# Kernel tuning notes

Hardware: AMD Instinct MI355X
Metric: run time of the kernel (lower is better)

Reference implementation:

```python
import jax, jax.numpy as jnp
import numpy as np

N = 50000          # nodes
E_RAND = 800000    # random edges (avg degree 16)
IN, HID, HEADS, OUT = 256, 64, 4, 40
NEG_SLOPE = 0.2    # PyG GATConv default leaky_relu slope
BN_EPS = 1e-5


def setup_inputs() -> dict:
    key = jax.random.key(0)
    ks = jax.random.split(key, 24)
    x = jax.random.normal(ks[0], (N, IN), jnp.float32)
    ei = jax.random.randint(ks[1], (2, E_RAND), 0, N)
    loops = jnp.arange(N, dtype=ei.dtype)
    edge_index = jnp.concatenate([ei, jnp.stack([loops, loops])], axis=1)  # add self loops (PyG default)
    s = 0.1
    d = {
        "x": x,
        "edge_index": edge_index,
        "W0": jax.random.normal(ks[2], (IN, HEADS * HID), jnp.float32) * s,
        "a_src0": jax.random.normal(ks[3], (HEADS, HID), jnp.float32) * s,
        "a_dst0": jax.random.normal(ks[4], (HEADS, HID), jnp.float32) * s,
        "b0": jax.random.normal(ks[5], (HEADS * HID,), jnp.float32) * s,
        "bn0_g": jnp.ones((HEADS * HID,), jnp.float32),
        "bn0_b": jnp.zeros((HEADS * HID,), jnp.float32),
        "bn0_m": jax.random.normal(ks[6], (HEADS * HID,), jnp.float32) * s,
        "bn0_v": jax.random.uniform(ks[7], (HEADS * HID,), jnp.float32, 0.5, 1.5),
        "W1": jax.random.normal(ks[8], (HEADS * HID, HEADS * HID), jnp.float32) * s,
        "a_src1": jax.random.normal(ks[9], (HEADS, HID), jnp.float32) * s,
        "a_dst1": jax.random.normal(ks[10], (HEADS, HID), jnp.float32) * s,
        "b1": jax.random.normal(ks[11], (HEADS * HID,), jnp.float32) * s,
        "bn1_g": jnp.ones((HEADS * HID,), jnp.float32),
        "bn1_b": jnp.zeros((HEADS * HID,), jnp.float32),
        "bn1_m": jax.random.normal(ks[12], (HEADS * HID,), jnp.float32) * s,
        "bn1_v": jax.random.uniform(ks[13], (HEADS * HID,), jnp.float32, 0.5, 1.5),
        "W2": jax.random.normal(ks[14], (HEADS * HID, OUT), jnp.float32) * s,
        "a_src2": jax.random.normal(ks[15], (1, OUT), jnp.float32) * s,
        "a_dst2": jax.random.normal(ks[16], (1, OUT), jnp.float32) * s,
        "b2": jax.random.normal(ks[17], (OUT,), jnp.float32) * s,
    }
    return d


def gat_conv(x, edge_index, W, att_src, att_dst, heads, ch):
    """PyG GATConv (eval mode): gather -> leaky_relu attn -> segment softmax -> scatter add."""
    src, dst = edge_index[0], edge_index[1]
    h = (x @ W).reshape(-1, heads, ch)                       # [N,H,C]
    a_s = jnp.einsum('nhc,hc->nh', h, att_src)
    a_d = jnp.einsum('nhc,hc->nh', h, att_dst)
    e = jax.nn.leaky_relu(a_s[src] + a_d[dst], NEG_SLOPE)    # [E,H]
    m = jax.ops.segment_max(e, dst, num_segments=N)
    m = jax.lax.stop_gradient(jnp.where(jnp.isfinite(m), m, 0.0))
    p = jnp.exp(e - m[dst])
    denom = jax.ops.segment_sum(p, dst, num_segments=N)
    alpha = p / (denom[dst] + 1e-16)                         # [E,H]
    msg = h[src] * alpha[:, :, None]                         # [E,H,C]
    return jax.ops.segment_sum(msg, dst, num_segments=N)     # [N,H,C]


def _bn(h, g, b, m, v):
    return g * (h - m) * jax.lax.rsqrt(v + BN_EPS) + b


def reference(x, edge_index, W0, a_src0, a_dst0, b0, bn0_g, bn0_b, bn0_m, bn0_v,
              W1, a_src1, a_dst1, b1, bn1_g, bn1_b, bn1_m, bn1_v,
              W2, a_src2, a_dst2, b2):
    h = gat_conv(x, edge_index, W0, a_src0, a_dst0, HEADS, HID).reshape(N, HEADS * HID) + b0
    h = jax.nn.elu(_bn(h, bn0_g, bn0_b, bn0_m, bn0_v))
    h = gat_conv(h, edge_index, W1, a_src1, a_dst1, HEADS, HID).reshape(N, HEADS * HID) + b1
    h = jax.nn.elu(_bn(h, bn1_g, bn1_b, bn1_m, bn1_v))
    out = gat_conv(h, edge_index, W2, a_src2, a_dst2, 1, OUT).reshape(N, OUT) + b2
    return out
```

## Files before the change

### kernel.cpp

```cpp
#include <hip/hip_runtime.h>
#include <cstdint>
#include <cstddef>

constexpr int kN = 50000;
constexpr float kSlope = 0.2f;
constexpr float kBnEps = 1e-5f;

static inline int ceil_div(int a, int b) { return (a + b - 1) / b; }

typedef __attribute__((ext_vector_type(8))) _Float16 half8;
typedef __attribute__((ext_vector_type(8))) unsigned short ushortx8;
typedef __attribute__((ext_vector_type(4))) float f32x4;

__device__ inline unsigned short f2h_us(float f) {
  _Float16 h = (_Float16)f;
  return *(unsigned short*)&h;
}

__device__ inline void gload16(const void* g, void* l) {
  __builtin_amdgcn_global_load_lds((const __attribute__((address_space(1))) unsigned int*)g,
                                   (__attribute__((address_space(3))) unsigned int*)l, 16, 0, 0);
}


__global__ void k_prep_degree(const int* __restrict__ dst, int* __restrict__ deg, int E,
                              const float* __restrict__ x, unsigned short* __restrict__ x16,
                              const float* __restrict__ W0, unsigned short* __restrict__ Wt0,
                              const float* __restrict__ W1, unsigned short* __restrict__ Wt1,
                              const float* __restrict__ W2, unsigned short* __restrict__ Wt2) {
  const int tid = blockIdx.x * blockDim.x + threadIdx.x;
  const int nthr = gridDim.x * blockDim.x;
  for (int e = tid; e < E; e += nthr) atomicAdd(&deg[dst[e]], 1);
  const int N4 = kN * 64;
  const int S0 = 256 * 256, S1 = 256 * 256, S2 = 128 * 256;
  const int total = N4 + S0 + S1 + S2;
  for (int i = tid; i < total; i += nthr) {
    if (i < N4) {
      float4 v = ((const float4*)x)[i];
      ushort4 o;
      o.x = f2h_us(v.x);
      o.y = f2h_us(v.y);
      o.z = f2h_us(v.z);
      o.w = f2h_us(v.w);
      ((ushort4*)x16)[i] = o;
    } else {
      int j = i - N4;
      if (j < S0) {
        int nc = j >> 8, k = j & 255;
        Wt0[j] = f2h_us(W0[(size_t)k * 256 + nc]);
      } else if (j < S0 + S1) {
        int t = j - S0;
        int nc = t >> 8, k = t & 255;
        Wt1[t] = f2h_us(W1[(size_t)k * 256 + nc]);
      } else {
        int t = j - S0 - S1;
        int nc = t >> 8, k = t & 255;
        Wt2[t] = (nc < 40) ? f2h_us(W2[(size_t)k * 40 + nc]) : (unsigned short)0;
      }
    }
  }
}


__global__ void k_scan1(const int* __restrict__ deg, int* __restrict__ rp,
                        int* __restrict__ bsum, int n) {
  __shared__ int sm[256];
  int i = blockIdx.x * 256 + threadIdx.x;
  int v = (i < n) ? deg[i] : 0;
  sm[threadIdx.x] = v;
  __syncthreads();
  for (int off = 1; off < 256; off <<= 1) {
    int t = (threadIdx.x >= off) ? sm[threadIdx.x - off] : 0;
    __syncthreads();
    sm[threadIdx.x] += t;
    __syncthreads();
  }
  if (i < n) rp[i + 1] = sm[threadIdx.x];
  if (threadIdx.x == 255) bsum[blockIdx.x] = sm[255];
}

__global__ void k_scan2(int* bsum, int nb) {
  __shared__ int sm[256];
  int v = (threadIdx.x < nb) ? bsum[threadIdx.x] : 0;
  sm[threadIdx.x] = v;
  __syncthreads();
  for (int off = 1; off < 256; off <<= 1) {
    int t = (threadIdx.x >= off) ? sm[threadIdx.x - off] : 0;
    __syncthreads();
    sm[threadIdx.x] += t;
    __syncthreads();
  }
  if (threadIdx.x < nb) bsum[threadIdx.x] = sm[threadIdx.x] - v;
}

__global__ void k_scan3(int* __restrict__ rp, const int* __restrict__ bsum, int n) {
  int i = blockIdx.x * 256 + threadIdx.x;
  if (i < n) rp[i + 1] += bsum[blockIdx.x];
  if (i == 0) rp[0] = 0;
}


__device__ __forceinline__ void gemm_body(
    int bx, int by, const unsigned short* __restrict__ A, const unsigned short* __restrict__ Bt,
    unsigned short* __restrict__ C, const float* __restrict__ asrc,
    const float* __restrict__ adst, float* __restrict__ a_s, float* __restrict__ a_d, int M,
    int K, int Nc, int ldc, int heads, int acols) {
  constexpr int BM = 128, BK = 32;
  __shared__ unsigned short As[BM * BK];
  __shared__ unsigned short Bs[BM * BK];
  int tid = threadIdx.x;
  int wave = tid >> 6, lane = tid & 63;
  int quad = lane >> 4, l16 = lane & 15;
  int wm = (wave & 1) * 64, wn = (wave >> 1) * 64;
  int bm = bx * BM, bn = by * BM;
  int srow = lane >> 2;
  int spart = lane & 3;
  f32x4 acc[4][4] = {};
  for (int k0 = 0; k0 < K; k0 += BK) {
#pragma unroll
    for (int it = 0; it < 2; it++) {
      int chunk = wave * 2 + it;
      int row = chunk * 16 + srow;
      gload16(A + (size_t)(bm + row) * K + k0 + spart * 8, As + chunk * 512);
      gload16(Bt + (size_t)(bn + row) * K + k0 + spart * 8, Bs + chunk * 512);
    }
    __syncthreads();
    half8 af[4], bf[4];
#pragma unroll
    for (int i = 0; i < 4; i++) {
      af[i] = *(const half8*)(As + (wm + i * 16 + l16) * BK + quad * 8);
      bf[i] = *(const half8*)(Bs + (wn + i * 16 + l16) * BK + quad * 8);
    }
#pragma unroll
    for (int i = 0; i < 4; i++)
#pragma unroll
      for (int j = 0; j < 4; j++)
        acc[i][j] = __builtin_amdgcn_mfma_f32_16x16x32_f16(af[i], bf[j], acc[i][j], 0, 0, 0);
    __syncthreads();
  }
#pragma unroll
  for (int i = 0; i < 4; i++) {
#pragma unroll
    for (int j = 0; j < 4; j++) {
      int col = bn + wn + j * 16 + l16;
      if (col >= Nc) continue;
#pragma unroll
      for (int r = 0; r < 4; r++) {
        int row = bm + wm + i * 16 + quad * 4 + r;
        if (row < M) C[(size_t)row * ldc + col] = f2h_us(acc[i][j][r]);
      }
    }
  }
  int ghead = (bn + wn) >> 6;
  if (ghead < heads) {
    float asv[4], adv[4];
#pragma unroll
    for (int j = 0; j < 4; j++) {
      int col = bn + wn + j * 16 + l16;
      bool ok = col < acols;
      asv[j] = ok ? asrc[col] : 0.f;
      adv[j] = ok ? adst[col] : 0.f;
    }
#pragma unroll
    for (int i = 0; i < 4; i++) {
#pragma unroll
      for (int r = 0; r < 4; r++) {
        float s = acc[i][0][r] * asv[0] + acc[i][1][r] * asv[1] + acc[i][2][r] * asv[2] +
                  acc[i][3][r] * asv[3];
        float d = acc[i][0][r] * adv[0] + acc[i][1][r] * adv[1] + acc[i][2][r] * adv[2] +
                  acc[i][3][r] * adv[3];
#pragma unroll
        for (int mask = 1; mask <= 8; mask <<= 1) {
          s += __shfl_xor(s, mask, 64);
          d += __shfl_xor(d, mask, 64);
        }
        if (l16 == 0) {
          int row = bm + wm + i * 16 + quad * 4 + r;
          if (row < M) {
            a_s[row * heads + ghead] = s;
            a_d[row * heads + ghead] = d;
          }
        }
      }
    }
  }
}

__global__ __launch_bounds__(256) void k_mfma_gemm(
    const unsigned short* __restrict__ A, const unsigned short* __restrict__ Bt,
    unsigned short* __restrict__ C, const float* __restrict__ asrc,
    const float* __restrict__ adst, float* __restrict__ a_s, float* __restrict__ a_d, int M,
    int K, int Nc, int ldc, int heads, int acols) {
  gemm_body(blockIdx.x, blockIdx.y, A, Bt, C, asrc, adst, a_s, a_d, M, K, Nc, ldc, heads, acols);
}


__global__ __launch_bounds__(256) void k_gemm0_scatter(
    const unsigned short* __restrict__ A, const unsigned short* __restrict__ Bt,
    unsigned short* __restrict__ C, const float* __restrict__ asrc,
    const float* __restrict__ adst, float* __restrict__ a_s, float* __restrict__ a_d, int M,
    int K, int gemmBlocks, const int* __restrict__ src, const int* __restrict__ dst,
    const int* __restrict__ rp, int* __restrict__ cur, int* __restrict__ csr, int E) {
  if ((int)blockIdx.x < gemmBlocks) {
    int bx = blockIdx.x >> 1, by = blockIdx.x & 1;
    gemm_body(bx, by, A, Bt, C, asrc, adst, a_s, a_d, M, K, 256, 256, 4, 256);
  } else {
    int e = (blockIdx.x - gemmBlocks) * 256 + threadIdx.x;
    if (e < E) {
      int d = dst[e];
      int pos = rp[d] + atomicAdd(&cur[d], 1);
      csr[pos] = src[e];
    }
  }
}


__global__ __launch_bounds__(256) void k_attn_agg256(
    const int* __restrict__ rp, const int* __restrict__ csr, const _Float16* __restrict__ h,
    const float* __restrict__ a_s, const float* __restrict__ a_d, const float* __restrict__ bias,
    const float* __restrict__ bg, const float* __restrict__ bb, const float* __restrict__ bm,
    const float* __restrict__ bv, unsigned short* __restrict__ out, int n_nodes) {
  int wid = (blockIdx.x * blockDim.x + threadIdx.x) >> 6;
  int lane = threadIdx.x & 63;
  if (wid >= n_nodes) return;
  int n = wid;
  int beg = rp[n], end = rp[n + 1];
  int half = lane >> 5, l32 = lane & 31;
  int head = l32 >> 3;
  int c = l32 * 8;
  float ad = a_d[n * 4 + head];
  float acc[8] = {};
  float psum = 0.f;
  int e = beg;
  for (; e + 8 <= end; e += 8) {
    int s0 = csr[e + half];
    int s1 = csr[e + 2 + half];
    int s2 = csr[e + 4 + half];
    int s3 = csr[e + 6 + half];
    float x0 = a_s[s0 * 4 + head] + ad;
    float x1 = a_s[s1 * 4 + head] + ad;
    float x2 = a_s[s2 * 4 + head] + ad;
    float x3 = a_s[s3 * 4 + head] + ad;
    half8 v0 = *(const half8*)(h + (size_t)s0 * 256 + c);
    half8 v1 = *(const half8*)(h + (size_t)s1 * 256 + c);
    half8 v2 = *(const half8*)(h + (size_t)s2 * 256 + c);
    half8 v3 = *(const half8*)(h + (size_t)s3 * 256 + c);
    x0 = x0 > 0.f ? x0 : x0 * kSlope;
    x1 = x1 > 0.f ? x1 : x1 * kSlope;
    x2 = x2 > 0.f ? x2 : x2 * kSlope;
    x3 = x3 > 0.f ? x3 : x3 * kSlope;
    float p0 = __expf(x0), p1 = __expf(x1);
    float p2 = __expf(x2), p3 = __expf(x3);
    psum += (p0 + p1) + (p2 + p3);
#pragma unroll
    for (int j = 0; j < 8; j++) {
      acc[j] += (float)v0[j] * p0 + (float)v1[j] * p1;
      acc[j] += (float)v2[j] * p2 + (float)v3[j] * p3;
    }
  }
  for (; e + 2 <= end; e += 2) {
    int s0 = csr[e + half];
    float x0 = a_s[s0 * 4 + head] + ad;
    x0 = x0 > 0.f ? x0 : x0 * kSlope;
    float p0 = __expf(x0);
    psum += p0;
    half8 v0 = *(const half8*)(h + (size_t)s0 * 256 + c);
#pragma unroll
    for (int j = 0; j < 8; j++) acc[j] += (float)v0[j] * p0;
  }
  if (e < end && half == 0) {
    int s0 = csr[e];
    float x0 = a_s[s0 * 4 + head] + ad;
    x0 = x0 > 0.f ? x0 : x0 * kSlope;
    float p0 = __expf(x0);
    psum += p0;
    half8 v0 = *(const half8*)(h + (size_t)s0 * 256 + c);
#pragma unroll
    for (int j = 0; j < 8; j++) acc[j] += (float)v0[j] * p0;
  }
  psum += __shfl_xor(psum, 32, 64);
#pragma unroll
  for (int j = 0; j < 8; j++) acc[j] += __shfl_xor(acc[j], 32, 64);
  if (half == 0) {
    float rden = 1.f / (psum + 1e-16f);
    ushortx8 o;
#pragma unroll
    for (int j = 0; j < 8; j++) {
      float v = acc[j] * rden + bias[c + j];
      v = bg[c + j] * (v - bm[c + j]) * rsqrtf(bv[c + j] + kBnEps) + bb[c + j];
      v = v > 0.f ? v : (__expf(v) - 1.f);
      o[j] = f2h_us(v);
    }
    *(ushortx8*)(out + (size_t)n * 256 + c) = o;
  }
}


__global__ __launch_bounds__(256) void k_attn_agg40(
    const int* __restrict__ rp, const int* __restrict__ csr, const _Float16* __restrict__ h,
    const float* __restrict__ a_s, const float* __restrict__ a_d, const float* __restrict__ bias,
    float* __restrict__ out, int n_nodes) {
  int wid = (blockIdx.x * blockDim.x + threadIdx.x) >> 6;
  int lane = threadIdx.x & 63;
  if (wid >= n_nodes) return;
  int n = wid;
  int beg = rp[n], end = rp[n + 1];
  float ad = a_d[n];
  int grp = lane >> 3, l8 = lane & 7;
  int c = l8 * 8;
  bool act = l8 < 5;
  float acc[8] = {};
  float psum = 0.f;
  for (int base = beg; base < end; base += 16) {
    int e0 = base + grp;
    int e1 = base + 8 + grp;
    if (e0 < end) {
      int s = csr[e0];
      float x = a_s[s] + ad;
      x = x > 0.f ? x : x * kSlope;
      float p = __expf(x);
      psum += p;
      if (act) {
        half8 hv = *(const half8*)(h + (size_t)s * 40 + c);
#pragma unroll
        for (int j = 0; j < 8; j++) acc[j] += (float)hv[j] * p;
      }
    }
    if (e1 < end) {
      int s = csr[e1];
      float x = a_s[s] + ad;
      x = x > 0.f ? x : x * kSlope;
      float p = __expf(x);
      psum += p;
      if (act) {
        half8 hv = *(const half8*)(h + (size_t)s * 40 + c);
#pragma unroll
        for (int j = 0; j < 8; j++) acc[j] += (float)hv[j] * p;
      }
    }
  }
#pragma unroll
  for (int mask = 8; mask <= 32; mask <<= 1) psum += __shfl_xor(psum, mask, 64);
#pragma unroll
  for (int j = 0; j < 8; j++) {
#pragma unroll
    for (int mask = 8; mask <= 32; mask <<= 1) acc[j] += __shfl_xor(acc[j], mask, 64);
  }
  if (lane < 5) {
    float rden = 1.f / (psum + 1e-16f);
    float4 o0, o1;
    o0.x = acc[0] * rden + bias[c + 0];
    o0.y = acc[1] * rden + bias[c + 1];
    o0.z = acc[2] * rden + bias[c + 2];
    o0.w = acc[3] * rden + bias[c + 3];
    o1.x = acc[4] * rden + bias[c + 4];
    o1.y = acc[5] * rden + bias[c + 5];
    o1.z = acc[6] * rden + bias[c + 6];
    o1.w = acc[7] * rden + bias[c + 7];
    *(float4*)(out + (size_t)n * 40 + c) = o0;
    *(float4*)(out + (size_t)n * 40 + c + 4) = o1;
  }
}


extern "C" void kernel_launch(void* const* d_in, const int* in_sizes, int n_in, void* d_out,
                              int out_size, void* d_ws, size_t ws_size, hipStream_t stream) {
  const float* x = (const float*)d_in[0];
  const int* ei = (const int*)d_in[1];
  const float* W0 = (const float*)d_in[2];
  const float* as0 = (const float*)d_in[3];
  const float* ad0 = (const float*)d_in[4];
  const float* b0 = (const float*)d_in[5];
  const float* bg0 = (const float*)d_in[6];
  const float* bb0 = (const float*)d_in[7];
  const float* bm0 = (const float*)d_in[8];
  const float* bv0 = (const float*)d_in[9];
  const float* W1 = (const float*)d_in[10];
  const float* as1 = (const float*)d_in[11];
  const float* ad1 = (const float*)d_in[12];
  const float* b1 = (const float*)d_in[13];
  const float* bg1 = (const float*)d_in[14];
  const float* bb1 = (const float*)d_in[15];
  const float* bm1 = (const float*)d_in[16];
  const float* bv1 = (const float*)d_in[17];
  const float* W2 = (const float*)d_in[18];
  const float* as2 = (const float*)d_in[19];
  const float* ad2 = (const float*)d_in[20];
  const float* b2 = (const float*)d_in[21];
  float* out = (float*)d_out;

  const int E = in_sizes[1] / 2;
  const int* srcIdx = ei;
  const int* dstIdx = ei + E;

  char* p = (char*)d_ws;
  auto alloc = [&](size_t bytes) -> void* {
    void* r = (void*)p;
    p += (bytes + 255) & ~(size_t)255;
    return r;
  };
  int* rp = (int*)alloc((kN + 1) * sizeof(int));
  int* degcur = (int*)alloc((size_t)2 * kN * sizeof(int));
  int* deg = degcur;
  int* cur = degcur + kN;
  int* bsum = (int*)alloc(256 * sizeof(int));
  int* csr = (int*)alloc((size_t)E * sizeof(int));
  float* a_s = (float*)alloc((size_t)kN * 4 * sizeof(float));
  float* a_d = (float*)alloc((size_t)kN * 4 * sizeof(float));
  unsigned short* x16 = (unsigned short*)alloc((size_t)kN * 256 * 2);
  unsigned short* h16 = (unsigned short*)alloc((size_t)kN * 256 * 2);
  unsigned short* act16 = (unsigned short*)alloc((size_t)kN * 256 * 2);
  unsigned short* Wt0 = (unsigned short*)alloc((size_t)256 * 256 * 2);
  unsigned short* Wt1 = (unsigned short*)alloc((size_t)256 * 256 * 2);
  unsigned short* Wt2 = (unsigned short*)alloc((size_t)128 * 256 * 2);

  const int nb = ceil_div(kN, 256);
  const int sblocks = ceil_div(E, 256);

  hipMemsetAsync(degcur, 0, (size_t)2 * kN * sizeof(int), stream);
  k_prep_degree<<<2048, 256, 0, stream>>>(dstIdx, deg, E, x, x16, W0, Wt0, W1, Wt1, W2, Wt2);
  k_scan1<<<nb, 256, 0, stream>>>(deg, rp, bsum, kN);
  k_scan2<<<1, 256, 0, stream>>>(bsum, nb);
  k_scan3<<<nb, 256, 0, stream>>>(rp, bsum, kN);

  const int gemmBlocks = ceil_div(kN, 128) * 2;
  k_gemm0_scatter<<<gemmBlocks + sblocks, 256, 0, stream>>>(
      x16, Wt0, h16, as0, ad0, a_s, a_d, kN, 256, gemmBlocks, srcIdx, dstIdx, rp, cur, csr, E);

  dim3 gg(ceil_div(kN, 128), 2);
  dim3 gg2(ceil_div(kN, 128), 1);
  int wpn_blocks = ceil_div(kN, 4);

  k_attn_agg256<<<wpn_blocks, 256, 0, stream>>>(rp, csr, (const _Float16*)h16, a_s, a_d, b0, bg0,
                                                bb0, bm0, bv0, act16, kN);

  k_mfma_gemm<<<gg, 256, 0, stream>>>(act16, Wt1, h16, as1, ad1, a_s, a_d, kN, 256, 256, 256, 4,
                                      256);
  k_attn_agg256<<<wpn_blocks, 256, 0, stream>>>(rp, csr, (const _Float16*)h16, a_s, a_d, b1, bg1,
                                                bb1, bm1, bv1, act16, kN);

  k_mfma_gemm<<<gg2, 256, 0, stream>>>(act16, Wt2, h16, as2, ad2, a_s, a_d, kN, 256, 40, 40, 1,
                                       40);
  k_attn_agg40<<<wpn_blocks, 256, 0, stream>>>(rp, csr, (const _Float16*)h16, a_s, a_d, b2, out,
                                               kN);
}
```

Baseline: 445.8 us.

## Fuse x fp32-to-fp16 conversion into layer-0 GEMM and widen GEMM tiles to full N

```diff
diff --git a/kernel.cpp b/kernel.cpp
--- a/kernel.cpp
+++ b/kernel.cpp
@@ -23,40 +23,27 @@
 }
 
 
-__global__ void k_prep_degree(const int* __restrict__ dst, int* __restrict__ deg, int E,
-                              const float* __restrict__ x, unsigned short* __restrict__ x16,
-                              const float* __restrict__ W0, unsigned short* __restrict__ Wt0,
-                              const float* __restrict__ W1, unsigned short* __restrict__ Wt1,
-                              const float* __restrict__ W2, unsigned short* __restrict__ Wt2) {
+__global__ void k_prepw_degree(const int* __restrict__ dst, int* __restrict__ deg, int E,
+                               const float* __restrict__ W0, unsigned short* __restrict__ Wt0,
+                               const float* __restrict__ W1, unsigned short* __restrict__ Wt1,
+                               const float* __restrict__ W2, unsigned short* __restrict__ Wt2) {
   const int tid = blockIdx.x * blockDim.x + threadIdx.x;
   const int nthr = gridDim.x * blockDim.x;
   for (int e = tid; e < E; e += nthr) atomicAdd(&deg[dst[e]], 1);
-  const int N4 = kN * 64;
   const int S0 = 256 * 256, S1 = 256 * 256, S2 = 128 * 256;
-  const int total = N4 + S0 + S1 + S2;
-  for (int i = tid; i < total; i += nthr) {
-    if (i < N4) {
-      float4 v = ((const float4*)x)[i];
-      ushort4 o;
-      o.x = f2h_us(v.x);
-      o.y = f2h_us(v.y);
-      o.z = f2h_us(v.z);
-      o.w = f2h_us(v.w);
-      ((ushort4*)x16)[i] = o;
+  const int total = S0 + S1 + S2;
+  for (int j = tid; j < total; j += nthr) {
+    if (j < S0) {
+      int nc = j >> 8, k = j & 255;
+      Wt0[j] = f2h_us(W0[(size_t)k * 256 + nc]);
+    } else if (j < S0 + S1) {
+      int t = j - S0;
+      int nc = t >> 8, k = t & 255;
+      Wt1[t] = f2h_us(W1[(size_t)k * 256 + nc]);
     } else {
-      int j = i - N4;
-      if (j < S0) {
-        int nc = j >> 8, k = j & 255;
-        Wt0[j] = f2h_us(W0[(size_t)k * 256 + nc]);
-      } else if (j < S0 + S1) {
-        int t = j - S0;
-        int nc = t >> 8, k = t & 255;
-        Wt1[t] = f2h_us(W1[(size_t)k * 256 + nc]);
-      } else {
-        int t = j - S0 - S1;
-        int nc = t >> 8, k = t & 255;
-        Wt2[t] = (nc < 40) ? f2h_us(W2[(size_t)k * 40 + nc]) : (unsigned short)0;
-      }
+      int t = j - S0 - S1;
+      int nc = t >> 8, k = t & 255;
+      Wt2[t] = (nc < 40) ? f2h_us(W2[(size_t)k * 40 + nc]) : (unsigned short)0;
     }
   }
 }
@@ -100,8 +87,145 @@
 }
 
 
-__device__ __forceinline__ void gemm_body(
-    int bx, int by, const unsigned short* __restrict__ A, const unsigned short* __restrict__ Bt,
+template <bool AF32>
+__device__ __forceinline__ void gemmN_body(int bx, const void* Av,
+                                           const unsigned short* __restrict__ Bt,
+                                           unsigned short* __restrict__ C,
+                                           const float* __restrict__ asrc,
+                                           const float* __restrict__ adst,
+                                           float* __restrict__ a_s, float* __restrict__ a_d,
+                                           int M) {
+  constexpr int BM = 128, BK = 32, K = 256;
+  __shared__ alignas(16) unsigned char AsRaw[BM * BK * 4];
+  __shared__ alignas(16) unsigned short Bs[256 * BK];
+  int tid = threadIdx.x;
+  int wave = tid >> 6, lane = tid & 63;
+  int quad = lane >> 4, l16 = lane & 15;
+  int wm = (wave & 1) * 64, wn = (wave >> 1) * 64;
+  int bm = bx * BM;
+  f32x4 acc[4][4] = {};
+  const float* Af = (const float*)Av;
+  const unsigned short* Ah = (const unsigned short*)Av;
+  for (int k0 = 0; k0 < K; k0 += BK) {
+#pragma unroll
+    for (int it = 0; it < 2; it++) {
+      int u = wave * 2 + it;
+      if (AF32) {
+        int row = u * 8 + (lane >> 3);
+        int part = lane & 7;
+        int gm = bm + row;
+        if (gm >= M) gm = M - 1;
+        gload16(Af + (size_t)gm * K + k0 + part * 4, AsRaw + u * 1024);
+      } else if (it == 0) {
+        int row = wave * 16 + (lane >> 2);
+        int part = lane & 3;
+        int gm = bm + row;
+        if (gm >= M) gm = M - 1;
+        gload16(Ah + (size_t)gm * K + k0 + part * 8, AsRaw + wave * 1024);
+      }
+      int brow = u * 16 + (lane >> 2);
+      int bpart = lane & 3;
+      gload16(Bt + (size_t)brow * K + k0 + bpart * 8, Bs + u * 512);
+    }
+    __syncthreads();
+    half8 af[4], bf[4];
+#pragma unroll
+    for (int i = 0; i < 4; i++) {
+      int arow = wm + i * 16 + l16;
+      if (AF32) {
+        const float4* As4 = (const float4*)AsRaw;
+        float4 lo = As4[arow * 8 + quad * 2];
+        float4 hi = As4[arow * 8 + quad * 2 + 1];
+        half8 a;
+        a[0] = (_Float16)lo.x; a[1] = (_Float16)lo.y;
+        a[2] = (_Float16)lo.z; a[3] = (_Float16)lo.w;
+        a[4] = (_Float16)hi.x; a[5] = (_Float16)hi.y;
+        a[6] = (_Float16)hi.z; a[7] = (_Float16)hi.w;
+        af[i] = a;
+      } else {
+        af[i] = *(const half8*)((const unsigned short*)AsRaw + arow * BK + quad * 8);
+      }
+      bf[i] = *(const half8*)(Bs + (wn + i * 16 + l16) * BK + quad * 8);
+    }
+#pragma unroll
+    for (int i = 0; i < 4; i++)
+#pragma unroll
+      for (int j = 0; j < 4; j++)
+        acc[i][j] = __builtin_amdgcn_mfma_f32_16x16x32_f16(af[i], bf[j], acc[i][j], 0, 0, 0);
+    __syncthreads();
+  }
+#pragma unroll
+  for (int i = 0; i < 4; i++) {
+#pragma unroll
+    for (int j = 0; j < 4; j++) {
+      int col = wn + j * 16 + l16;
+#pragma unroll
+      for (int r = 0; r < 4; r++) {
+        int row = bm + wm + i * 16 + quad * 4 + r;
+        if (row < M) C[(size_t)row * 256 + col] = f2h_us(acc[i][j][r]);
+      }
+    }
+  }
+  int ghead = wn >> 6;
+  float asv[4], adv[4];
+#pragma unroll
+  for (int j = 0; j < 4; j++) {
+    int col = wn + j * 16 + l16;
+    asv[j] = asrc[col];
+    adv[j] = adst[col];
+  }
+#pragma unroll
+  for (int i = 0; i < 4; i++) {
+#pragma unroll
+    for (int r = 0; r < 4; r++) {
+      float s = acc[i][0][r] * asv[0] + acc[i][1][r] * asv[1] + acc[i][2][r] * asv[2] +
+                acc[i][3][r] * asv[3];
+      float d = acc[i][0][r] * adv[0] + acc[i][1][r] * adv[1] + acc[i][2][r] * adv[2] +
+                acc[i][3][r] * adv[3];
+#pragma unroll
+      for (int mask = 1; mask <= 8; mask <<= 1) {
+        s += __shfl_xor(s, mask, 64);
+        d += __shfl_xor(d, mask, 64);
+      }
+      if (l16 == 0) {
+        int row = bm + wm + i * 16 + quad * 4 + r;
+        if (row < M) {
+          a_s[row * 4 + ghead] = s;
+          a_d[row * 4 + ghead] = d;
+        }
+      }
+    }
+  }
+}
+
+__global__ __launch_bounds__(512) void k_gemmN_f16(
+    const unsigned short* __restrict__ A, const unsigned short* __restrict__ Bt,
+    unsigned short* __restrict__ C, const float* __restrict__ asrc,
+    const float* __restrict__ adst, float* __restrict__ a_s, float* __restrict__ a_d, int M) {
+  gemmN_body<false>(blockIdx.x, A, Bt, C, asrc, adst, a_s, a_d, M);
+}
+
+__global__ __launch_bounds__(512) void k_gemm0_scatter(
+    const float* __restrict__ A, const unsigned short* __restrict__ Bt,
+    unsigned short* __restrict__ C, const float* __restrict__ asrc,
+    const float* __restrict__ adst, float* __restrict__ a_s, float* __restrict__ a_d, int M,
+    int gemmBlocks, const int* __restrict__ src, const int* __restrict__ dst,
+    const int* __restrict__ rp, int* __restrict__ cur, int* __restrict__ csr, int E) {
+  if ((int)blockIdx.x < gemmBlocks) {
+    gemmN_body<true>(blockIdx.x, A, Bt, C, asrc, adst, a_s, a_d, M);
+  } else {
+    int e = (blockIdx.x - gemmBlocks) * 512 + threadIdx.x;
+    if (e < E) {
+      int d = dst[e];
+      int pos = rp[d] + atomicAdd(&cur[d], 1);
+      csr[pos] = src[e];
+    }
+  }
+}
+
+
+__global__ __launch_bounds__(256) void k_mfma_gemm(
+    const unsigned short* __restrict__ A, const unsigned short* __restrict__ Bt,
     unsigned short* __restrict__ C, const float* __restrict__ asrc,
     const float* __restrict__ adst, float* __restrict__ a_s, float* __restrict__ a_d, int M,
     int K, int Nc, int ldc, int heads, int acols) {
@@ -112,7 +236,7 @@
   int wave = tid >> 6, lane = tid & 63;
   int quad = lane >> 4, l16 = lane & 15;
   int wm = (wave & 1) * 64, wn = (wave >> 1) * 64;
-  int bm = bx * BM, bn = by * BM;
+  int bm = blockIdx.x * BM, bn = blockIdx.y * BM;
   int srow = lane >> 2;
   int spart = lane & 3;
   f32x4 acc[4][4] = {};
@@ -182,34 +306,6 @@
           }
         }
       }
-    }
-  }
-}
-
-__global__ __launch_bounds__(256) void k_mfma_gemm(
-    const unsigned short* __restrict__ A, const unsigned short* __restrict__ Bt,
-    unsigned short* __restrict__ C, const float* __restrict__ asrc,
-    const float* __restrict__ adst, float* __restrict__ a_s, float* __restrict__ a_d, int M,
-    int K, int Nc, int ldc, int heads, int acols) {
-  gemm_body(blockIdx.x, blockIdx.y, A, Bt, C, asrc, adst, a_s, a_d, M, K, Nc, ldc, heads, acols);
-}
-
-
-__global__ __launch_bounds__(256) void k_gemm0_scatter(
-    const unsigned short* __restrict__ A, const unsigned short* __restrict__ Bt,
-    unsigned short* __restrict__ C, const float* __restrict__ asrc,
-    const float* __restrict__ adst, float* __restrict__ a_s, float* __restrict__ a_d, int M,
-    int K, int gemmBlocks, const int* __restrict__ src, const int* __restrict__ dst,
-    const int* __restrict__ rp, int* __restrict__ cur, int* __restrict__ csr, int E) {
-  if ((int)blockIdx.x < gemmBlocks) {
-    int bx = blockIdx.x >> 1, by = blockIdx.x & 1;
-    gemm_body(bx, by, A, Bt, C, asrc, adst, a_s, a_d, M, K, 256, 256, 4, 256);
-  } else {
-    int e = (blockIdx.x - gemmBlocks) * 256 + threadIdx.x;
-    if (e < E) {
-      int d = dst[e];
-      int pos = rp[d] + atomicAdd(&cur[d], 1);
-      csr[pos] = src[e];
     }
   }
 }
@@ -407,7 +503,6 @@
   int* csr = (int*)alloc((size_t)E * sizeof(int));
   float* a_s = (float*)alloc((size_t)kN * 4 * sizeof(float));
   float* a_d = (float*)alloc((size_t)kN * 4 * sizeof(float));
-  unsigned short* x16 = (unsigned short*)alloc((size_t)kN * 256 * 2);
   unsigned short* h16 = (unsigned short*)alloc((size_t)kN * 256 * 2);
   unsigned short* act16 = (unsigned short*)alloc((size_t)kN * 256 * 2);
   unsigned short* Wt0 = (unsigned short*)alloc((size_t)256 * 256 * 2);
@@ -415,27 +510,25 @@
   unsigned short* Wt2 = (unsigned short*)alloc((size_t)128 * 256 * 2);
 
   const int nb = ceil_div(kN, 256);
-  const int sblocks = ceil_div(E, 256);
 
   hipMemsetAsync(degcur, 0, (size_t)2 * kN * sizeof(int), stream);
-  k_prep_degree<<<2048, 256, 0, stream>>>(dstIdx, deg, E, x, x16, W0, Wt0, W1, Wt1, W2, Wt2);
+  k_prepw_degree<<<1024, 256, 0, stream>>>(dstIdx, deg, E, W0, Wt0, W1, Wt1, W2, Wt2);
   k_scan1<<<nb, 256, 0, stream>>>(deg, rp, bsum, kN);
   k_scan2<<<1, 256, 0, stream>>>(bsum, nb);
   k_scan3<<<nb, 256, 0, stream>>>(rp, bsum, kN);
 
-  const int gemmBlocks = ceil_div(kN, 128) * 2;
-  k_gemm0_scatter<<<gemmBlocks + sblocks, 256, 0, stream>>>(
-      x16, Wt0, h16, as0, ad0, a_s, a_d, kN, 256, gemmBlocks, srcIdx, dstIdx, rp, cur, csr, E);
-
-  dim3 gg(ceil_div(kN, 128), 2);
+  const int gemmBlocks = ceil_div(kN, 128);
+  const int sblocks = ceil_div(E, 512);
+  k_gemm0_scatter<<<gemmBlocks + sblocks, 512, 0, stream>>>(
+      x, Wt0, h16, as0, ad0, a_s, a_d, kN, gemmBlocks, srcIdx, dstIdx, rp, cur, csr, E);
+
+  int wpn_blocks = ceil_div(kN, 4);
   dim3 gg2(ceil_div(kN, 128), 1);
-  int wpn_blocks = ceil_div(kN, 4);
 
   k_attn_agg256<<<wpn_blocks, 256, 0, stream>>>(rp, csr, (const _Float16*)h16, a_s, a_d, b0, bg0,
                                                 bb0, bm0, bv0, act16, kN);
 
-  k_mfma_gemm<<<gg, 256, 0, stream>>>(act16, Wt1, h16, as1, ad1, a_s, a_d, kN, 256, 256, 256, 4,
-                                      256);
+  k_gemmN_f16<<<gemmBlocks, 512, 0, stream>>>(act16, Wt1, h16, as1, ad1, a_s, a_d, kN);
   k_attn_agg256<<<wpn_blocks, 256, 0, stream>>>(rp, csr, (const _Float16*)h16, a_s, a_d, b1, bg1,
                                                 bb1, bm1, bv1, act16, kN);
 
```

Result: no change. 449.5 us (+0.8%).
